# Kernel optimization log

Hardware: AMD Instinct MI355X
Metric: run time of the kernel (lower is better)

## Reference

```python
import jax, jax.numpy as jnp
import numpy as np

D_MODEL = 512
NUM_HEADS = 8


def setup_inputs() -> dict:
    key = jax.random.key(0)
    ks = jax.random.split(key, 6)
    B, S, D = 4, 2048, D_MODEL
    Q = jax.random.normal(ks[0], (B, S, D), dtype=jnp.float32)
    K = jax.random.normal(ks[1], (B, S, D), dtype=jnp.float32)
    V = jax.random.normal(ks[2], (B, S, D), dtype=jnp.float32)
    # boolean mask, True = masked out; random so no row is fully masked
    mask = jax.random.randint(ks[3], (B, S, S), 0, 2).astype(jnp.bool_)
    scale = 1.0 / np.sqrt(D)
    Wq = jax.random.normal(ks[4], (D, D), dtype=jnp.float32) * scale
    Wo = jax.random.normal(ks[5], (D, D), dtype=jnp.float32) * scale
    return {"Q": Q, "K": K, "V": V, "mask": mask, "Wq": Wq, "Wo": Wo}


def reference(Q, K, V, mask, Wq, Wo):
    B, S, D = Q.shape
    H = NUM_HEADS
    dk = D // H
    # Faithful to the source: Q_Linear's weight (Wq) is applied to Q, K AND V
    # (K_Linear / V_Linear are dead parameters in the original module).
    q = (Q @ Wq.T).reshape(B, S, H, dk)
    k = (K @ Wq.T).reshape(B, S, H, dk)
    v = (V @ Wq.T).reshape(B, S, H, dk)
    # scores: [B, H, Sq, Sk]
    scores = jnp.einsum("bqhd,bkhd->bhqk", q, k)
    scores = jnp.where(mask[:, None, :, :], -jnp.inf, scores)
    w = jax.nn.softmax(scores / jnp.sqrt(jnp.asarray(dk, scores.dtype)), axis=-1)
    c = jnp.einsum("bhqk,bkhd->bqhd", w, v).reshape(B, S, D)
    return c @ Wo.T
```

## Files before the change

kernel.cpp:

```cpp
#include <hip/hip_runtime.h>
#include <math.h>

#define B_ 4
#define S_ 2048
#define D_ 512
#define H_ 8
#define DK_ 64
#define MROWS (B_ * S_)

typedef short bf16x8 __attribute__((ext_vector_type(8)));
typedef float f32x4 __attribute__((ext_vector_type(4)));

static __device__ __forceinline__ unsigned short f2bf(float x) {
    unsigned int u = __float_as_uint(x);
    return (unsigned short)((u + 0x7FFFu + ((u >> 16) & 1u)) >> 16);
}
static __device__ __forceinline__ unsigned int cvt_pk_bf16(float a, float b) {
    unsigned int r;
    asm("v_cvt_pk_bf16_f32 %0, %1, %2" : "=v"(r) : "v"(a), "v"(b));
    return r;
}
static __device__ __forceinline__ float exp2_fast(float x) {
    float r;
    asm("v_exp_f32 %0, %1" : "=v"(r) : "v"(x));
    return r;
}

#define NXE (MROWS * D_)
#define NWE (D_ * D_)
#define CAST_BLOCKS ((3 * NXE + 2 * NWE) / 8 / 256)
#define MASK_BLOCKS (B_ * S_ * S_ / 256)

__global__ __launch_bounds__(256) void prep(const float* __restrict__ Q,
                                            const float* __restrict__ K,
                                            const float* __restrict__ V,
                                            const float* __restrict__ Wq,
                                            const float* __restrict__ Wo,
                                            const void* __restrict__ mask,
                                            unsigned short* __restrict__ Qb,
                                            unsigned short* __restrict__ Kb,
                                            unsigned short* __restrict__ Vb,
                                            unsigned short* __restrict__ Wqb,
                                            unsigned short* __restrict__ Wob,
                                            unsigned long long* __restrict__ mb) {
    if (blockIdx.x < CAST_BLOCKS) {
        const int NA = NXE / 8;
        const int NWn = NWE / 8;
        int id = blockIdx.x * 256 + threadIdx.x;
        const float* src;
        unsigned short* dst;
        if (id < 3 * NA) {
            int a = id / NA, r = id - a * NA;
            src = (a == 0 ? Q : a == 1 ? K : V) + (size_t)r * 8;
            dst = (a == 0 ? Qb : a == 1 ? Kb : Vb) + (size_t)r * 8;
        } else {
            int r = id - 3 * NA;
            int a = r / NWn; r -= a * NWn;
            src = (a == 0 ? Wq : Wo) + (size_t)r * 8;
            dst = (a == 0 ? Wqb : Wob) + (size_t)r * 8;
        }
        float4 x = *(const float4*)src;
        float4 y = *(const float4*)(src + 4);
        unsigned short u[8] = {f2bf(x.x), f2bf(x.y), f2bf(x.z), f2bf(x.w),
                               f2bf(y.x), f2bf(y.y), f2bf(y.z), f2bf(y.w)};
        *(uint4*)dst = *(const uint4*)u;
    } else {
        const int id = (blockIdx.x - CAST_BLOCKS) * 256 + threadIdx.x;
        unsigned int accw = 0;
        if ((threadIdx.x & 63) == 0) {
            const unsigned int* mw0 = (const unsigned int*)mask;
            #pragma unroll
            for (int i = 0; i < 16; ++i) accw |= mw0[i];
        }
        accw = __shfl(accw, 0);
        const bool bytemode = (accw & 0xFFFFFF00u) != 0u;
        int val;
        if (bytemode) val = ((const unsigned char*)mask)[id];
        else          val = ((const int*)mask)[id];
        unsigned long long w = __ballot(val != 0);
        if ((threadIdx.x & 63) == 0) mb[id >> 6] = w;
    }
}

__global__ __launch_bounds__(256) void proj3(const unsigned short* __restrict__ Qb,
                                             const unsigned short* __restrict__ Kb,
                                             const unsigned short* __restrict__ Vb,
                                             const unsigned short* __restrict__ Wqb,
                                             unsigned short* __restrict__ qs,
                                             unsigned short* __restrict__ kbo,
                                             unsigned short* __restrict__ vt) {
    __shared__ unsigned short As[128 * 40];
    __shared__ unsigned short Bs[128 * 40];
    const int t = threadIdx.x;
    const int w = t >> 6, lane = t & 63, col = lane & 15, quad = lane >> 4;
    const int bm = blockIdx.x * 128, bn = blockIdx.y * 128;
    const int z = blockIdx.z;
    const unsigned short* X = (z == 0) ? Qb : (z == 1) ? Kb : Vb;
    const int wm = (w >> 1) * 64, wn = (w & 1) * 64;
    const int srow = t >> 1, shalf = t & 1;

    const unsigned short* xg = X + (size_t)(bm + srow) * D_ + shalf * 16;
    const unsigned short* wg = Wqb + (size_t)(bn + srow) * D_ + shalf * 16;
    unsigned short* asw = &As[srow * 40 + shalf * 16];
    unsigned short* bsw = &Bs[srow * 40 + shalf * 16];

    f32x4 acc[4][4];
    #pragma unroll
    for (int i = 0; i < 4; ++i)
        #pragma unroll
        for (int j = 0; j < 4; ++j) acc[i][j] = (f32x4){0.f, 0.f, 0.f, 0.f};

    #pragma unroll 1
    for (int k0 = 0; k0 < D_; k0 += 32) {
        __syncthreads();
        {
            uint4 a0 = *(const uint4*)(xg + k0);
            uint4 a1 = *(const uint4*)(xg + k0 + 8);
            uint4 b0 = *(const uint4*)(wg + k0);
            uint4 b1 = *(const uint4*)(wg + k0 + 8);
            *(uint4*)asw = a0; *(uint4*)(asw + 8) = a1;
            *(uint4*)bsw = b0; *(uint4*)(bsw + 8) = b1;
        }
        __syncthreads();

        bf16x8 af[4], bg[4];
        #pragma unroll
        for (int i = 0; i < 4; ++i)
            af[i] = *(const bf16x8*)&As[(wm + i * 16 + col) * 40 + quad * 8];
        #pragma unroll
        for (int j = 0; j < 4; ++j)
            bg[j] = *(const bf16x8*)&Bs[(wn + j * 16 + col) * 40 + quad * 8];
        #pragma unroll
        for (int i = 0; i < 4; ++i)
            #pragma unroll
            for (int j = 0; j < 4; ++j)
                acc[i][j] = __builtin_amdgcn_mfma_f32_16x16x32_bf16(
                    af[i], bg[j], acc[i][j], 0, 0, 0);
    }

    if (z == 2) {
        #pragma unroll
        for (int i = 0; i < 4; ++i) {
            const int R = bm + wm + i * 16 + quad * 4;
            const int bb = R >> 11, s0 = R & (S_ - 1);
            #pragma unroll
            for (int j = 0; j < 4; ++j) {
                const int C = bn + wn + j * 16 + col;
                const int hh = C >> 6, dd = C & (DK_ - 1);
                ushort4 u = make_ushort4(f2bf(acc[i][j][0]), f2bf(acc[i][j][1]),
                                         f2bf(acc[i][j][2]), f2bf(acc[i][j][3]));
                *(ushort4*)&vt[(((size_t)bb * H_ + hh) * DK_ + dd) * S_ + s0] = u;
            }
        }
    } else {
        unsigned short* O = (z == 0) ? qs : kbo;
        const float scl = (z == 0) ? 0.18033688f : 1.0f;
        #pragma unroll
        for (int i = 0; i < 4; ++i)
            #pragma unroll
            for (int j = 0; j < 4; ++j) {
                const int R = bm + wm + i * 16 + quad * 4;
                const int C = bn + wn + j * 16 + col;
                #pragma unroll
                for (int r = 0; r < 4; ++r)
                    O[(size_t)(R + r) * D_ + C] = f2bf(acc[i][j][r] * scl);
            }
    }
}

__global__ __launch_bounds__(256) void gemm_out(const unsigned short* __restrict__ Xb,
                                                const unsigned short* __restrict__ Wob,
                                                float* __restrict__ Out) {
    __shared__ unsigned short As[128 * 40];
    __shared__ unsigned short Bs[128 * 40];
    const int t = threadIdx.x;
    const int w = t >> 6, lane = t & 63, col = lane & 15, quad = lane >> 4;
    const int bm = blockIdx.x * 128, bn = blockIdx.y * 128;
    const int wm = (w >> 1) * 64, wn = (w & 1) * 64;
    const int srow = t >> 1, shalf = t & 1;

    const unsigned short* xg = Xb + (size_t)(bm + srow) * D_ + shalf * 16;
    const unsigned short* wg = Wob + (size_t)(bn + srow) * D_ + shalf * 16;
    unsigned short* asw = &As[srow * 40 + shalf * 16];
    unsigned short* bsw = &Bs[srow * 40 + shalf * 16];

    f32x4 acc[4][4];
    #pragma unroll
    for (int i = 0; i < 4; ++i)
        #pragma unroll
        for (int j = 0; j < 4; ++j) acc[i][j] = (f32x4){0.f, 0.f, 0.f, 0.f};

    #pragma unroll 1
    for (int k0 = 0; k0 < D_; k0 += 32) {
        __syncthreads();
        {
            uint4 a0 = *(const uint4*)(xg + k0);
            uint4 a1 = *(const uint4*)(xg + k0 + 8);
            uint4 b0 = *(const uint4*)(wg + k0);
            uint4 b1 = *(const uint4*)(wg + k0 + 8);
            *(uint4*)asw = a0; *(uint4*)(asw + 8) = a1;
            *(uint4*)bsw = b0; *(uint4*)(bsw + 8) = b1;
        }
        __syncthreads();

        bf16x8 af[4], bg[4];
        #pragma unroll
        for (int i = 0; i < 4; ++i)
            af[i] = *(const bf16x8*)&As[(wm + i * 16 + col) * 40 + quad * 8];
        #pragma unroll
        for (int j = 0; j < 4; ++j)
            bg[j] = *(const bf16x8*)&Bs[(wn + j * 16 + col) * 40 + quad * 8];
        #pragma unroll
        for (int i = 0; i < 4; ++i)
            #pragma unroll
            for (int j = 0; j < 4; ++j)
                acc[i][j] = __builtin_amdgcn_mfma_f32_16x16x32_bf16(
                    af[i], bg[j], acc[i][j], 0, 0, 0);
    }

    #pragma unroll
    for (int i = 0; i < 4; ++i)
        #pragma unroll
        for (int j = 0; j < 4; ++j) {
            const int R = bm + wm + i * 16 + quad * 4;
            const int C = bn + wn + j * 16 + col;
            #pragma unroll
            for (int r = 0; r < 4; ++r)
                Out[(size_t)(R + r) * D_ + C] = acc[i][j][r];
        }
}

__global__ __launch_bounds__(256, 4) void attn_mfma(
        const unsigned short* __restrict__ qb,
        const unsigned short* __restrict__ kb,
        const unsigned short* __restrict__ vt,
        const unsigned long long* __restrict__ mb,
        unsigned short* __restrict__ o0,
        unsigned short* __restrict__ o1,
        float* __restrict__ l0,
        float* __restrict__ l1) {
    __shared__ unsigned short sm[18432];
    const int t = threadIdx.x;
    const int w = t >> 6;
    const int lane = t & 63;
    const int col = lane & 15;
    const int quad = lane >> 4;
    const int h = blockIdx.y;
    const int b = blockIdx.z >> 1;
    const int khalf = blockIdx.z & 1;
    const int bh = b * H_ + h;
    const int qrow0 = blockIdx.x * 128 + w * 32;

    unsigned short* opart = khalf ? o1 : o0;
    float* lpart = khalf ? l1 : l0;

    const int KS = 0;
    const int VS = 4608;
    const int PS = 9216 + w * 2304;

    const unsigned int chk = cvt_pk_bf16(1.0f, 2.0f);
    const int dlo = ((chk & 0xFFFFu) == 0x3F80u) ? 0 : 16;
    const int dhi = 16 - dlo;

    bf16x8 aQ0[2], aQ1[2];
    #pragma unroll
    for (int s = 0; s < 2; ++s) {
        const unsigned short* qp =
            qb + (size_t)(b * S_ + qrow0 + s * 16 + col) * D_ + h * DK_ + quad * 8;
        aQ0[s] = *(const bf16x8*)(qp);
        aQ1[s] = *(const bf16x8*)(qp + 32);
    }

    bf16x8 ones;
    #pragma unroll
    for (int i = 0; i < 8; ++i) ones[i] = (short)0x3F80;

    f32x4 O[2][4];
    #pragma unroll
    for (int s = 0; s < 2; ++s)
        #pragma unroll
        for (int g = 0; g < 4; ++g) O[s][g] = (f32x4){0.f, 0.f, 0.f, 0.f};
    f32x4 lacc[2];
    lacc[0] = (f32x4){0.f, 0.f, 0.f, 0.f};
    lacc[1] = (f32x4){0.f, 0.f, 0.f, 0.f};

    const int trow = t >> 2;
    const int tseg = (t & 3) * 16;
    const unsigned short* kgp = kb + (size_t)(b * S_ + trow) * D_ + h * DK_ + tseg;
    const unsigned short* vgp = vt + ((size_t)bh * DK_ + trow) * S_ + tseg;
    unsigned short* ksw = &sm[KS + trow * 72 + tseg];
    unsigned short* vsw = &sm[VS + trow * 72 + tseg];

    const float CREF = 8.656170245f;
    const int kbeg = khalf * (S_ / 2);

    #pragma unroll 1
    for (int k0 = kbeg; k0 < kbeg + S_ / 2; k0 += 64) {
        __syncthreads();
        {
            const unsigned short* g1 = kgp + (size_t)k0 * D_;
            uint4 ka0 = *(const uint4*)g1;
            uint4 ka1 = *(const uint4*)(g1 + 8);
            const unsigned short* g2 = vgp + k0;
            uint4 vb0 = *(const uint4*)g2;
            uint4 vb1 = *(const uint4*)(g2 + 8);
            *(uint4*)ksw = ka0; *(uint4*)(ksw + 8) = ka1;
            *(uint4*)vsw = vb0; *(uint4*)(vsw + 8) = vb1;
        }
        __syncthreads();

        f32x4 sc[2][4];
        #pragma unroll
        for (int g = 0; g < 4; ++g) {
            bf16x8 bk0 = *(const bf16x8*)&sm[KS + (g * 16 + col) * 72 + quad * 8];
            bf16x8 bk1 = *(const bf16x8*)&sm[KS + (g * 16 + col) * 72 + 32 + quad * 8];
            #pragma unroll
            for (int s = 0; s < 2; ++s) {
                f32x4 z = {0.f, 0.f, 0.f, 0.f};
                z = __builtin_amdgcn_mfma_f32_16x16x32_bf16(aQ0[s], bk0, z, 0, 0, 0);
                z = __builtin_amdgcn_mfma_f32_16x16x32_bf16(aQ1[s], bk1, z, 0, 0, 0);
                sc[s][g] = z;
            }
        }

        #pragma unroll
        for (int s = 0; s < 2; ++s) {
            unsigned long long mw[4];
            #pragma unroll
            for (int r = 0; r < 4; ++r)
                mw[r] = mb[(size_t)(b * S_ + qrow0 + s * 16 + quad * 4 + r) * (S_ / 64)
                           + (k0 >> 6)];
            #pragma unroll
            for (int r = 0; r < 4; ++r) {
                const unsigned long long sh = mw[r] >> col;
                const unsigned int lo = (unsigned int)sh;
                const unsigned int hi = (unsigned int)(sh >> 32);
                float p0 = exp2_fast(((lo & 1u)       ? -1e30f : sc[s][0][r]) - CREF);
                float p1 = exp2_fast(((lo & 0x10000u) ? -1e30f : sc[s][1][r]) - CREF);
                float p2 = exp2_fast(((hi & 1u)       ? -1e30f : sc[s][2][r]) - CREF);
                float p3 = exp2_fast(((hi & 0x10000u) ? -1e30f : sc[s][3][r]) - CREF);
                const unsigned int u01 = cvt_pk_bf16(p0, p1);
                const unsigned int u23 = cvt_pk_bf16(p2, p3);
                const int prow = PS + (s * 16 + quad * 4 + r) * 72 + col;
                sm[prow + dlo]      = (unsigned short)u01;
                sm[prow + dhi]      = (unsigned short)(u01 >> 16);
                sm[prow + 32 + dlo] = (unsigned short)u23;
                sm[prow + 32 + dhi] = (unsigned short)(u23 >> 16);
            }
        }
        __asm__ __volatile__("s_waitcnt lgkmcnt(0)" ::: "memory");

        bf16x8 aP0[2], aP1[2];
        #pragma unroll
        for (int s = 0; s < 2; ++s) {
            aP0[s] = *(const bf16x8*)&sm[PS + (s * 16 + col) * 72 + quad * 8];
            aP1[s] = *(const bf16x8*)&sm[PS + (s * 16 + col) * 72 + 32 + quad * 8];
        }

        #pragma unroll
        for (int s = 0; s < 2; ++s) {
            lacc[s] = __builtin_amdgcn_mfma_f32_16x16x32_bf16(aP0[s], ones, lacc[s], 0, 0, 0);
            lacc[s] = __builtin_amdgcn_mfma_f32_16x16x32_bf16(aP1[s], ones, lacc[s], 0, 0, 0);
        }

        #pragma unroll
        for (int g = 0; g < 4; ++g) {
            bf16x8 bv0 = *(const bf16x8*)&sm[VS + (g * 16 + col) * 72 + quad * 8];
            bf16x8 bv1 = *(const bf16x8*)&sm[VS + (g * 16 + col) * 72 + 32 + quad * 8];
            #pragma unroll
            for (int s = 0; s < 2; ++s) {
                O[s][g] = __builtin_amdgcn_mfma_f32_16x16x32_bf16(aP0[s], bv0, O[s][g], 0, 0, 0);
                O[s][g] = __builtin_amdgcn_mfma_f32_16x16x32_bf16(aP1[s], bv1, O[s][g], 0, 0, 0);
            }
        }
    }

    #pragma unroll
    for (int s = 0; s < 2; ++s)
        #pragma unroll
        for (int r = 0; r < 4; ++r) {
            const int row = b * S_ + qrow0 + s * 16 + quad * 4 + r;
            #pragma unroll
            for (int g = 0; g < 4; ++g)
                opart[(size_t)row * D_ + h * DK_ + g * 16 + col] = f2bf(O[s][g][r]);
            if (col == 0) lpart[(size_t)row * H_ + h] = lacc[s][r];
        }
}

__global__ __launch_bounds__(256) void combine(const unsigned short* __restrict__ o0,
                                               const unsigned short* __restrict__ o1,
                                               const float* __restrict__ l0,
                                               const float* __restrict__ l1,
                                               unsigned short* __restrict__ cb) {
    const int id = blockIdx.x * 256 + threadIdx.x;
    const size_t base = (size_t)id * 8;
    const int row = (int)(base >> 9);
    const int hh = ((int)base & (D_ - 1)) >> 6;
    uint4 ua = *(const uint4*)(o0 + base);
    uint4 ub = *(const uint4*)(o1 + base);
    const float inv = 1.0f / (l0[(size_t)row * H_ + hh] + l1[(size_t)row * H_ + hh]);
    const unsigned short* pa = (const unsigned short*)&ua;
    const unsigned short* pb = (const unsigned short*)&ub;
    unsigned short out[8];
    #pragma unroll
    for (int i = 0; i < 8; ++i) {
        float fa = __uint_as_float((unsigned int)pa[i] << 16);
        float fb = __uint_as_float((unsigned int)pb[i] << 16);
        out[i] = f2bf((fa + fb) * inv);
    }
    *(uint4*)(cb + base) = *(const uint4*)out;
}

extern "C" void kernel_launch(void* const* d_in, const int* in_sizes, int n_in,
                              void* d_out, int out_size, void* d_ws, size_t ws_size,
                              hipStream_t stream) {
    const float* Q    = (const float*)d_in[0];
    const float* K    = (const float*)d_in[1];
    const float* V    = (const float*)d_in[2];
    const void*  mask = d_in[3];
    const float* Wq   = (const float*)d_in[4];
    const float* Wo   = (const float*)d_in[5];
    float* out = (float*)d_out;

    const size_t NX = (size_t)MROWS * D_;
    const size_t NW = (size_t)D_ * D_;
    unsigned short* Qb   = (unsigned short*)d_ws;
    unsigned short* Kb   = Qb + NX;
    unsigned short* Vb   = Kb + NX;
    unsigned short* Wqb  = Vb + NX;
    unsigned short* Wob  = Wqb + NW;
    unsigned short* qbuf = Wob + NW;
    unsigned short* kbuf = qbuf + NX;
    unsigned short* vtb  = kbuf + NX;
    unsigned short* cbuf = vtb + NX;
    unsigned long long* mb = (unsigned long long*)(cbuf + NX);

    unsigned short* o0 = Qb;
    unsigned short* o1 = Kb;
    float* l0 = (float*)Vb;
    float* l1 = l0 + (size_t)MROWS * H_;

    prep<<<dim3(CAST_BLOCKS + MASK_BLOCKS), dim3(256), 0, stream>>>(
        Q, K, V, Wq, Wo, mask, Qb, Kb, Vb, Wqb, Wob, mb);

    proj3<<<dim3(MROWS / 128, D_ / 128, 3), dim3(256), 0, stream>>>(
        Qb, Kb, Vb, Wqb, qbuf, kbuf, vtb);

    attn_mfma<<<dim3(S_ / 128, H_, B_ * 2), dim3(256), 0, stream>>>(
        qbuf, kbuf, vtb, mb, o0, o1, l0, l1);

    combine<<<dim3((int)(NX / 8 / 256)), dim3(256), 0, stream>>>(o0, o1, l0, l1, cbuf);

    gemm_out<<<dim3(MROWS / 128, D_ / 128), dim3(256), 0, stream>>>(cbuf, Wob, out);
}
```

Measured before the change: 279.5 us.

## Double-buffer K/V tiles via direct global-to-LDS loads with XOR swizzle

Replaces the synchronous register-staged K/V tile loads with asynchronous global_load_lds into a double-buffered, XOR-swizzled LDS layout. The next tile and its mask words are prefetched while the current tile is computed, with explicit vmcnt waits and raw barriers. It also raises wave priority around the MFMA blocks. Occupancy drops from 4 to 3 blocks per CU because of the larger LDS footprint, and correctness depends on the hand-counted vmcnt value and the barrier ordering.

```diff
diff --git a/kernel.cpp b/kernel.cpp
--- a/kernel.cpp
+++ b/kernel.cpp
@@ -24,6 +24,11 @@
     float r;
     asm("v_exp_f32 %0, %1" : "=v"(r) : "v"(x));
     return r;
+}
+static __device__ __forceinline__ void gld_lds16(const unsigned short* g, unsigned short* l) {
+    __builtin_amdgcn_global_load_lds(
+        (const __attribute__((address_space(1))) unsigned int*)g,
+        (__attribute__((address_space(3))) unsigned int*)l, 16, 0, 0);
 }
 
 #define NXE (MROWS * D_)
@@ -230,7 +235,7 @@
         }
 }
 
-__global__ __launch_bounds__(256, 4) void attn_mfma(
+__global__ __launch_bounds__(256, 3) void attn_mfma(
         const unsigned short* __restrict__ qb,
         const unsigned short* __restrict__ kb,
         const unsigned short* __restrict__ vt,
@@ -239,7 +244,7 @@
         unsigned short* __restrict__ o1,
         float* __restrict__ l0,
         float* __restrict__ l1) {
-    __shared__ unsigned short sm[18432];
+    __shared__ unsigned short sm[25600];
     const int t = threadIdx.x;
     const int w = t >> 6;
     const int lane = t & 63;
@@ -254,9 +259,7 @@
     unsigned short* opart = khalf ? o1 : o0;
     float* lpart = khalf ? l1 : l0;
 
-    const int KS = 0;
-    const int VS = 4608;
-    const int PS = 9216 + w * 2304;
+    const int PS = 16384 + w * 2304;
 
     const unsigned int chk = cvt_pk_bf16(1.0f, 2.0f);
     const int dlo = ((chk & 0xFFFFu) == 0x3F80u) ? 0 : 16;
@@ -284,36 +287,67 @@
     lacc[0] = (f32x4){0.f, 0.f, 0.f, 0.f};
     lacc[1] = (f32x4){0.f, 0.f, 0.f, 0.f};
 
-    const int trow = t >> 2;
-    const int tseg = (t & 3) * 16;
-    const unsigned short* kgp = kb + (size_t)(b * S_ + trow) * D_ + h * DK_ + tseg;
-    const unsigned short* vgp = vt + ((size_t)bh * DK_ + trow) * S_ + tseg;
-    unsigned short* ksw = &sm[KS + trow * 72 + tseg];
-    unsigned short* vsw = &sm[VS + trow * 72 + tseg];
-
     const float CREF = 8.656170245f;
     const int kbeg = khalf * (S_ / 2);
 
+    const int ln8 = lane >> 3;
+    const int fs8 = ((lane & 7) ^ ln8) * 8;
+    const int r0 = w * 16 + ln8;
+    const unsigned short* pK0 = kb + (size_t)(b * S_ + kbeg + r0) * D_ + h * DK_ + fs8;
+    const unsigned short* pK1 = pK0 + 8 * D_;
+    const unsigned short* pV0 = vt + ((size_t)bh * DK_ + r0) * S_ + kbeg + fs8;
+    const unsigned short* pV1 = pV0 + 8 * S_;
+
+    const unsigned long long* mbase =
+        mb + (size_t)(b * S_ + qrow0 + quad * 4) * (S_ / 64) + (kbeg >> 6);
+
+    gld_lds16(pK0, &sm[w * 1024]);
+    gld_lds16(pK1, &sm[w * 1024 + 512]);
+    gld_lds16(pV0, &sm[4096 + w * 1024]);
+    gld_lds16(pV1, &sm[4096 + w * 1024 + 512]);
+    pK0 += 64 * D_; pK1 += 64 * D_; pV0 += 64; pV1 += 64;
+
+    unsigned long long mc[8];
+    #pragma unroll
+    for (int s = 0; s < 2; ++s)
+        #pragma unroll
+        for (int r = 0; r < 4; ++r)
+            mc[s * 4 + r] = mbase[(s * 16 + r) * 32];
+
+    const int ps0 = (quad ^ (col & 7)) * 8;
+    const int ps1 = ps0 ^ 32;
+
     #pragma unroll 1
-    for (int k0 = kbeg; k0 < kbeg + S_ / 2; k0 += 64) {
-        __syncthreads();
-        {
-            const unsigned short* g1 = kgp + (size_t)k0 * D_;
-            uint4 ka0 = *(const uint4*)g1;
-            uint4 ka1 = *(const uint4*)(g1 + 8);
-            const unsigned short* g2 = vgp + k0;
-            uint4 vb0 = *(const uint4*)g2;
-            uint4 vb1 = *(const uint4*)(g2 + 8);
-            *(uint4*)ksw = ka0; *(uint4*)(ksw + 8) = ka1;
-            *(uint4*)vsw = vb0; *(uint4*)(vsw + 8) = vb1;
-        }
-        __syncthreads();
+    for (int ti = 0; ti < 16; ++ti) {
+        unsigned long long mn[8];
+        if (ti < 15) {
+            const int nb = (ti & 1) ? 0 : 8192;
+            gld_lds16(pK0, &sm[nb + w * 1024]);
+            gld_lds16(pK1, &sm[nb + w * 1024 + 512]);
+            gld_lds16(pV0, &sm[nb + 4096 + w * 1024]);
+            gld_lds16(pV1, &sm[nb + 4096 + w * 1024 + 512]);
+            pK0 += 64 * D_; pK1 += 64 * D_; pV0 += 64; pV1 += 64;
+            #pragma unroll
+            for (int s = 0; s < 2; ++s)
+                #pragma unroll
+                for (int r = 0; r < 4; ++r)
+                    mn[s * 4 + r] = mbase[(s * 16 + r) * 32 + ti + 1];
+            __asm__ __volatile__("s_waitcnt vmcnt(12)" ::: "memory");
+        } else {
+            __asm__ __volatile__("s_waitcnt vmcnt(0)" ::: "memory");
+        }
+        __builtin_amdgcn_s_barrier();
+
+        const int KB = (ti & 1) ? 8192 : 0;
+        const int VB = KB + 4096;
 
         f32x4 sc[2][4];
+        __builtin_amdgcn_s_setprio(1);
         #pragma unroll
         for (int g = 0; g < 4; ++g) {
-            bf16x8 bk0 = *(const bf16x8*)&sm[KS + (g * 16 + col) * 72 + quad * 8];
-            bf16x8 bk1 = *(const bf16x8*)&sm[KS + (g * 16 + col) * 72 + 32 + quad * 8];
+            const int krow = KB + (g * 16 + col) * 64;
+            bf16x8 bk0 = *(const bf16x8*)&sm[krow + ps0];
+            bf16x8 bk1 = *(const bf16x8*)&sm[krow + ps1];
             #pragma unroll
             for (int s = 0; s < 2; ++s) {
                 f32x4 z = {0.f, 0.f, 0.f, 0.f};
@@ -322,17 +356,13 @@
                 sc[s][g] = z;
             }
         }
+        __builtin_amdgcn_s_setprio(0);
 
         #pragma unroll
         for (int s = 0; s < 2; ++s) {
-            unsigned long long mw[4];
-            #pragma unroll
-            for (int r = 0; r < 4; ++r)
-                mw[r] = mb[(size_t)(b * S_ + qrow0 + s * 16 + quad * 4 + r) * (S_ / 64)
-                           + (k0 >> 6)];
             #pragma unroll
             for (int r = 0; r < 4; ++r) {
-                const unsigned long long sh = mw[r] >> col;
+                const unsigned long long sh = mc[s * 4 + r] >> col;
                 const unsigned int lo = (unsigned int)sh;
                 const unsigned int hi = (unsigned int)(sh >> 32);
                 float p0 = exp2_fast(((lo & 1u)       ? -1e30f : sc[s][0][r]) - CREF);
@@ -357,6 +387,7 @@
             aP1[s] = *(const bf16x8*)&sm[PS + (s * 16 + col) * 72 + 32 + quad * 8];
         }
 
+        __builtin_amdgcn_s_setprio(1);
         #pragma unroll
         for (int s = 0; s < 2; ++s) {
             lacc[s] = __builtin_amdgcn_mfma_f32_16x16x32_bf16(aP0[s], ones, lacc[s], 0, 0, 0);
@@ -365,13 +396,21 @@
 
         #pragma unroll
         for (int g = 0; g < 4; ++g) {
-            bf16x8 bv0 = *(const bf16x8*)&sm[VS + (g * 16 + col) * 72 + quad * 8];
-            bf16x8 bv1 = *(const bf16x8*)&sm[VS + (g * 16 + col) * 72 + 32 + quad * 8];
+            const int vrow = VB + (g * 16 + col) * 64;
+            bf16x8 bv0 = *(const bf16x8*)&sm[vrow + ps0];
+            bf16x8 bv1 = *(const bf16x8*)&sm[vrow + ps1];
             #pragma unroll
             for (int s = 0; s < 2; ++s) {
                 O[s][g] = __builtin_amdgcn_mfma_f32_16x16x32_bf16(aP0[s], bv0, O[s][g], 0, 0, 0);
                 O[s][g] = __builtin_amdgcn_mfma_f32_16x16x32_bf16(aP1[s], bv1, O[s][g], 0, 0, 0);
             }
+        }
+        __builtin_amdgcn_s_setprio(0);
+
+        if (ti < 15) {
+            #pragma unroll
+            for (int i = 0; i < 8; ++i) mc[i] = mn[i];
+            __builtin_amdgcn_s_barrier();
         }
     }
 
```

Measured after the change: 288.7 us. +3.3%, slower.
